# Performance work log

Measured on AMD Instinct MI355X. Metric: run time of the kernel, lower is better.

Reference implementation:

```python
import jax, jax.numpy as jnp
import numpy as np

N, D, K = 500_000, 64, 512

def setup_inputs() -> dict:
    key = jax.random.key(0)
    k1, k2, k3 = jax.random.split(key, 3)
    X = jax.random.normal(k1, (N, D), dtype=jnp.float32)
    centroids = jax.random.normal(k2, (K, D), dtype=jnp.float32)
    sample_weight = jax.random.uniform(k3, (N, D), dtype=jnp.float32)
    return {"X": X, "centroids": centroids, "sample_weight": sample_weight}

def reference(X, centroids, sample_weight):
    k, d = centroids.shape
    XX = jnp.sum(X * X, axis=1, keepdims=True)              # (N,1)
    CC = jnp.sum(centroids * centroids, axis=1)[None, :]    # (1,K)  == _centroid_sum
    Xc = X @ centroids.T                                    # (N,K)
    distances = jnp.sqrt(jnp.clip(XX - 2.0 * Xc + CC, 0.0) / d)
    y_hat = jnp.argmin(distances, axis=1)                   # hard assignment
    inertia = jnp.sum(jnp.min(distances, axis=1))           # summarize() return value
    # scatter_add_ accumulation of sufficient statistics
    w_sum = jax.ops.segment_sum(sample_weight, y_hat, num_segments=k)        # (K,D)
    xw_sum = jax.ops.segment_sum(X * sample_weight, y_hat, num_segments=k)   # (K,D)
    # pack outputs into a single array: rows [0:K]=xw_sum, [K:2K]=w_sum, last row=inertia
    return jnp.concatenate([xw_sum, w_sum, jnp.broadcast_to(inertia / d, (1, d)) * 0 + inertia[None if False else ...] if False else jnp.broadcast_to(inertia, (1, d))], axis=0)
```

## Files before the change

kernel.cpp:

```cpp
#include <hip/hip_runtime.h>
#include <hip/hip_bf16.h>


#define D_DIM 64
#define K_CLUS 512
#define RPT 128
#define AGRID_MAX 1024
#define SEGROWS 64

typedef __attribute__((ext_vector_type(8))) short short8;
typedef __attribute__((ext_vector_type(4))) float f32x4;

__device__ inline void barrier_lds_only() {
    asm volatile("s_waitcnt lgkmcnt(0)\n\ts_barrier" ::: "memory");
}

__device__ inline float dot4sq(float4 a) {
    return a.x * a.x + a.y * a.y + a.z * a.z + a.w * a.w;
}
__device__ inline unsigned short bfb(float f) {
    unsigned int u = __float_as_uint(f);
    return (unsigned short)((u + 0x7FFFu + ((u >> 16) & 1u)) >> 16);
}
__device__ inline short8 pack8f(float4 a, float4 b) {
    union { short8 s; __hip_bfloat162 q[4]; } r;
    r.q[0] = __float22bfloat162_rn(make_float2(a.x, a.y));
    r.q[1] = __float22bfloat162_rn(make_float2(a.z, a.w));
    r.q[2] = __float22bfloat162_rn(make_float2(b.x, b.y));
    r.q[3] = __float22bfloat162_rn(make_float2(b.z, b.w));
    return r.s;
}
__device__ inline float bfhi(unsigned u) { return __uint_as_float(u & 0xFFFF0000u); }
__device__ inline float bflo(unsigned u) { return __uint_as_float(u << 16); }

__global__ void cc_kernel(const float* __restrict__ C, float* __restrict__ CChalf,
                          unsigned short* __restrict__ Cb, int k_total) {
    int k = blockIdx.x * blockDim.x + threadIdx.x;
    if (k >= k_total) return;
    const float4* cp = (const float4*)(C + (size_t)k * D_DIM);
    unsigned short* ob = Cb + (size_t)k * D_DIM;
    float s = 0.f;
#pragma unroll
    for (int i = 0; i < 16; ++i) {
        float4 c = cp[i];
        s += dot4sq(c);
        ob[4 * i + 0] = bfb(c.x); ob[4 * i + 1] = bfb(c.y);
        ob[4 * i + 2] = bfb(c.z); ob[4 * i + 3] = bfb(c.w);
    }
    CChalf[k] = 0.5f * s;
}

__global__ __launch_bounds__(512, 4) void assign_mfma(
        const float* __restrict__ X, const unsigned short* __restrict__ Cb,
        const float* __restrict__ CChalf, int* __restrict__ y,
        int* __restrict__ lrank, int* __restrict__ baseTab,
        int* __restrict__ count, float* __restrict__ inertia_ws,
        uint4* __restrict__ X16, int n, int ntiles) {
    __shared__ __align__(16) char xb_lds[RPT * 128];
    __shared__ __align__(16) unsigned int partial[RPT][8];
    __shared__ float xs_lds[2][RPT];
    __shared__ int lhist[K_CLUS];

    int tid = threadIdx.x;
    lhist[tid] = 0;

    int lane = tid & 63, wid = tid >> 6;
    int c15 = lane & 15, g = lane >> 4;
    int wbase = wid * 64;

    short8 cf0[4], cf1[4];
    f32x4 nc[4];
#pragma unroll
    for (int ct = 0; ct < 4; ++ct) {
        const char* cp = (const char*)(Cb + (size_t)(wbase + ct * 16 + c15) * D_DIM);
        cf0[ct] = *(const short8*)(cp + (g << 4));
        cf1[ct] = *(const short8*)(cp + 64 + (g << 4));
#pragma unroll
        for (int r2 = 0; r2 < 4; ++r2)
            nc[ct][r2] = -CChalf[wbase + ct * 16 + (g << 2) + r2];
    }

    int srow = tid >> 3;
    int sb = (tid & 7) << 4;
    int sf = (tid & 7) << 3;
    unsigned swz = ((unsigned)(srow & 7)) << 4;

    float4 a0 = {0,0,0,0}, a1 = {0,0,0,0}, b0 = {0,0,0,0}, b1 = {0,0,0,0};
    int tile = blockIdx.x;
    if (tile < ntiles) {
        int rA = min(tile * RPT + srow, n - 1);
        int rB = min(tile * RPT + 64 + srow, n - 1);
        const float4* xa = (const float4*)(X + (size_t)rA * D_DIM + sf);
        const float4* xb = (const float4*)(X + (size_t)rB * D_DIM + sf);
        a0 = xa[0]; a1 = xa[1]; b0 = xb[0]; b1 = xb[1];
    }
    float iner = 0.f;
    int it = 0;

    for (; tile < ntiles; tile += gridDim.x, ++it) {
        int par = it & 1;
        int rA = min(tile * RPT + srow, n - 1);
        int rB = min(tile * RPT + 64 + srow, n - 1);
        short8 pA = pack8f(a0, a1);
        short8 pB = pack8f(b0, b1);
        *(short8*)(xb_lds + (srow << 7) + (sb ^ swz)) = pA;
        *(short8*)(xb_lds + ((64 + srow) << 7) + (sb ^ swz)) = pB;
        float psA = dot4sq(a0) + dot4sq(a1);
        float psB = dot4sq(b0) + dot4sq(b1);
        psA += __shfl_xor(psA, 1); psA += __shfl_xor(psA, 2); psA += __shfl_xor(psA, 4);
        psB += __shfl_xor(psB, 1); psB += __shfl_xor(psB, 2); psB += __shfl_xor(psB, 4);
        if ((tid & 7) == 0) {
            xs_lds[par][srow] = psA;
            xs_lds[par][64 + srow] = psB;
        }
        barrier_lds_only();

        union { short8 s8; uint4 u4; } cA, cB;
        cA.s8 = pA; cB.s8 = pB;
        X16[(size_t)rA * 8 + (tid & 7)] = cA.u4;
        X16[(size_t)rB * 8 + (tid & 7)] = cB.u4;

        int ntile = tile + gridDim.x;
        if (ntile < ntiles) {
            int nA = min(ntile * RPT + srow, n - 1);
            int nB = min(ntile * RPT + 64 + srow, n - 1);
            const float4* xa = (const float4*)(X + (size_t)nA * D_DIM + sf);
            const float4* xb = (const float4*)(X + (size_t)nB * D_DIM + sf);
            a0 = xa[0]; a1 = xa[1]; b0 = xb[0]; b1 = xb[1];
        }

#pragma unroll
        for (int s = 0; s < 8; ++s) {
            int arow = s * 16 + c15;
            const char* ab = xb_lds + (arow << 7);
            unsigned asw = ((unsigned)(arow & 7)) << 4;
            short8 xa = *(const short8*)(ab + ((g << 4) ^ asw));
            short8 xbv = *(const short8*)(ab + ((64 + (g << 4)) ^ asw));

            float best = -3.4e38f;
            int bpos = 0;
#pragma unroll
            for (int ct = 0; ct < 4; ++ct) {
                f32x4 acc = __builtin_amdgcn_mfma_f32_16x16x32_bf16(cf0[ct], xa, nc[ct], 0, 0, 0);
                acc = __builtin_amdgcn_mfma_f32_16x16x32_bf16(cf1[ct], xbv, acc, 0, 0, 0);
                float sc0 = acc[0], sc1 = acc[1], sc2 = acc[2], sc3 = acc[3];
                bool b01 = sc1 > sc0;  float v01 = b01 ? sc1 : sc0;  int p01 = b01 ? 1 : 0;
                bool b23 = sc3 > sc2;  float v23 = b23 ? sc3 : sc2;  int p23 = b23 ? 3 : 2;
                bool bq  = v23 > v01;  float vq  = bq ? v23 : v01;   int pq  = bq ? p23 : p01;
                if (vq > best) { best = vq; bpos = (ct << 2) + pq; }
            }
            int kg = wbase + ((bpos >> 2) << 4) + (g << 2) + (bpos & 3);
            unsigned u = __float_as_uint(best);
            unsigned mono = u ^ ((u & 0x80000000u) ? 0xFFFFFFFFu : 0x80000000u);
            unsigned key = (mono & 0xFFFFFE00u) | ((unsigned)kg ^ 0x1FFu);
            unsigned o = (unsigned)__shfl_xor((int)key, 16); key = key > o ? key : o;
            o = (unsigned)__shfl_xor((int)key, 32); key = key > o ? key : o;
            if (g == 0) partial[s * 16 + c15][wid] = key;
        }
        barrier_lds_only();

        if (tid < RPT) {
            int grow = tile * RPT + tid;
            if (grow < n) {
                const uint4* pp = (const uint4*)&partial[tid][0];
                uint4 p0 = pp[0], p1 = pp[1];
                unsigned key = p0.x;
                key = key > p0.y ? key : p0.y;
                key = key > p0.z ? key : p0.z;
                key = key > p0.w ? key : p0.w;
                key = key > p1.x ? key : p1.x;
                key = key > p1.y ? key : p1.y;
                key = key > p1.z ? key : p1.z;
                key = key > p1.w ? key : p1.w;
                int kg = (int)((key & 0x1FFu) ^ 0x1FFu);
                unsigned m2 = (key & 0xFFFFFE00u) | 0x100u;
                unsigned ub = (m2 & 0x80000000u) ? (m2 ^ 0x80000000u) : ~m2;
                float sbest = __uint_as_float(ub);
                float xx = xs_lds[par][tid];
                y[grow] = kg;
                lrank[grow] = atomicAdd(&lhist[kg], 1);
                iner += sqrtf(fmaxf(xx - 2.f * sbest, 0.f) * (1.0f / 64.0f));
            }
        }
    }

    __syncthreads();
    int b = atomicAdd(count + tid, lhist[tid]);
    baseTab[blockIdx.x * K_CLUS + tid] = b;

    if (wid < 2) {
#pragma unroll
        for (int off = 1; off < 64; off <<= 1) iner += __shfl_xor(iner, off);
        if (lane == 0) atomicAdd(inertia_ws, iner);
    }
}

__global__ __launch_bounds__(K_CLUS) void prefix_kernel(
        const int* __restrict__ count, int* __restrict__ offset,
        int* __restrict__ segKS, int* __restrict__ segmeta) {
    __shared__ int tmp[K_CLUS];
    __shared__ int tns[K_CLUS];
    int t = threadIdx.x;
    int c = count[t];
    int ns = (c + SEGROWS - 1) / SEGROWS;
    tmp[t] = c; tns[t] = ns;
    __syncthreads();
    for (int s = 1; s < K_CLUS; s <<= 1) {
        int v1 = (t >= s) ? tmp[t - s] : 0;
        int v2 = (t >= s) ? tns[t - s] : 0;
        __syncthreads();
        tmp[t] += v1; tns[t] += v2;
        __syncthreads();
    }
    offset[t] = tmp[t] - c;
    int so = tns[t] - ns;
    for (int s = 0; s < ns; ++s) segKS[so + s] = (t << 16) | s;
    if (t == K_CLUS - 1) segmeta[0] = tns[t];
}

__global__ __launch_bounds__(256) void scatter_kernel(
        const int* __restrict__ y, const int* __restrict__ lrank,
        const int* __restrict__ offset, const int* __restrict__ baseTab,
        int* __restrict__ sorted, int n, int agrid) {
    int row = blockIdx.x * blockDim.x + threadIdx.x;
    if (row >= n) return;
    int k = y[row];
    int blk = (row / RPT) % agrid;
    sorted[offset[k] + baseTab[blk * K_CLUS + k] + lrank[row]] = row;
}

__global__ __launch_bounds__(256, 6) void cluster_accum_v3(
        const uint4* __restrict__ X16, const float* __restrict__ W,
        const int* __restrict__ sorted, const int* __restrict__ offset,
        const int* __restrict__ count, const int* __restrict__ segKS,
        const int* __restrict__ segmeta, float* __restrict__ out) {
    int bid = blockIdx.x;
    if (bid >= segmeta[0]) return;
    int v = segKS[bid];
    int k = v >> 16, s = v & 0xFFFF;
    int cnt = count[k];
    int lo = s * SEGROWS;
    int m = min(cnt - lo, SEGROWS);
    int start = offset[k] + lo;
    int lane = threadIdx.x & 63, w = threadIdx.x >> 6;
    int grp = (w << 2) | (lane >> 4);
    int l8 = lane & 7;
    int h = (lane >> 3) & 1;
    int g4 = grp * 4;
    const float4* W4 = (const float4*)W;

    int i0 = g4 + h;
    int i1 = g4 + 2 + h;
    int r0 = (i0 < m) ? sorted[start + i0] : -1;
    int r1 = (i1 < m) ? sorted[start + i1] : -1;

    uint4 zz = {0u, 0u, 0u, 0u};
    float4 fz = {0.f, 0.f, 0.f, 0.f};
    uint4 xq0 = zz, xq1 = zz;
    float4 wa0 = fz, wb0 = fz, wa1 = fz, wb1 = fz;
    if (r0 >= 0) {
        xq0 = X16[(size_t)r0 * 8 + l8];
        wa0 = W4[(size_t)r0 * 16 + 2 * l8];
        wb0 = W4[(size_t)r0 * 16 + 2 * l8 + 1];
    }
    if (r1 >= 0) {
        xq1 = X16[(size_t)r1 * 8 + l8];
        wa1 = W4[(size_t)r1 * 16 + 2 * l8];
        wb1 = W4[(size_t)r1 * 16 + 2 * l8 + 1];
    }

    float axw[8], aww[8];
#pragma unroll
    for (int j = 0; j < 8; ++j) { axw[j] = 0.f; aww[j] = 0.f; }

#pragma unroll
    for (int r = 0; r < 2; ++r) {
        uint4 xq = r ? xq1 : xq0;
        float4 wa = r ? wa1 : wa0;
        float4 wb = r ? wb1 : wb0;
        float xf[8];
        xf[0] = bflo(xq.x); xf[1] = bfhi(xq.x);
        xf[2] = bflo(xq.y); xf[3] = bfhi(xq.y);
        xf[4] = bflo(xq.z); xf[5] = bfhi(xq.z);
        xf[6] = bflo(xq.w); xf[7] = bfhi(xq.w);
        axw[0] = fmaf(xf[0], wa.x, axw[0]); aww[0] += wa.x;
        axw[1] = fmaf(xf[1], wa.y, axw[1]); aww[1] += wa.y;
        axw[2] = fmaf(xf[2], wa.z, axw[2]); aww[2] += wa.z;
        axw[3] = fmaf(xf[3], wa.w, axw[3]); aww[3] += wa.w;
        axw[4] = fmaf(xf[4], wb.x, axw[4]); aww[4] += wb.x;
        axw[5] = fmaf(xf[5], wb.y, axw[5]); aww[5] += wb.y;
        axw[6] = fmaf(xf[6], wb.z, axw[6]); aww[6] += wb.z;
        axw[7] = fmaf(xf[7], wb.w, axw[7]); aww[7] += wb.w;
    }
#pragma unroll
    for (int j = 0; j < 8; ++j) {
        axw[j] += __shfl_xor(axw[j], 8);
        aww[j] += __shfl_xor(aww[j], 8);
    }

    __shared__ float sxw[16][D_DIM];
    __shared__ float sww[16][D_DIM];
    if (h == 0) {
#pragma unroll
        for (int j = 0; j < 8; ++j) {
            sxw[grp][8 * l8 + j] = axw[j];
            sww[grp][8 * l8 + j] = aww[j];
        }
    }
    __syncthreads();
    int t = threadIdx.x;
    if (t < 128) {
        int half = t >> 6, d = t & 63;
        const float(*src)[D_DIM] = half ? sww : sxw;
        float acc = 0.f;
#pragma unroll
        for (int jg = 0; jg < 16; ++jg) acc += src[jg][d];
        atomicAdd(out + (size_t)(half ? K_CLUS + k : k) * D_DIM + d, acc);
    }
}

__global__ void finalize_kernel(const float* __restrict__ inertia_ws, float* __restrict__ out) {
    out[(size_t)(2 * K_CLUS) * D_DIM + threadIdx.x] = *inertia_ws;
}

__global__ __launch_bounds__(256) void assign_scalar(
        const float* __restrict__ X, const float* __restrict__ C,
        const float* __restrict__ CChalf, int* __restrict__ y,
        int* __restrict__ count, float* __restrict__ inertia_ws, int n) {
    int row = blockIdx.x * blockDim.x + threadIdx.x;
    float mind = 0.f;
    if (row < n) {
        float4 x[16];
        const float4* xp = (const float4*)(X + (size_t)row * D_DIM);
#pragma unroll
        for (int i = 0; i < 16; ++i) x[i] = xp[i];
        float xx = 0.f;
#pragma unroll
        for (int i = 0; i < 16; ++i) xx += dot4sq(x[i]);
        float best = -3.4e38f;
        int bestk = 0;
        for (int k = 0; k < K_CLUS; ++k) {
            const float4* cp = (const float4*)(C + (size_t)k * D_DIM);
            float s0 = 0.f;
#pragma unroll
            for (int i = 0; i < 16; ++i) {
                float4 c = cp[i];
                s0 += x[i].x * c.x + x[i].y * c.y + x[i].z * c.z + x[i].w * c.w;
            }
            float sc = s0 - CChalf[k];
            if (sc > best) { best = sc; bestk = k; }
        }
        y[row] = bestk;
        atomicAdd(&count[bestk], 1);
        mind = sqrtf(fmaxf(xx - 2.f * best, 0.f) * (1.0f / 64.0f));
    }
    float s = mind;
#pragma unroll
    for (int off = 32; off > 0; off >>= 1) s += __shfl_xor(s, off);
    __shared__ float wsum[4];
    int w = threadIdx.x >> 6;
    if ((threadIdx.x & 63) == 0) wsum[w] = s;
    __syncthreads();
    if (threadIdx.x == 0)
        atomicAdd(inertia_ws, wsum[0] + wsum[1] + wsum[2] + wsum[3]);
}

__global__ __launch_bounds__(256) void accum_atomic_kernel(
        const float* __restrict__ X, const float* __restrict__ W,
        const int* __restrict__ y, float* __restrict__ out, int n) {
    int row = blockIdx.x * blockDim.x + threadIdx.x;
    if (row >= n) return;
    int k = y[row];
    const float4* xp = (const float4*)(X + (size_t)row * D_DIM);
    const float4* wp = (const float4*)(W + (size_t)row * D_DIM);
    float* xw = out + (size_t)k * D_DIM;
    float* wsv = out + (size_t)(K_CLUS + k) * D_DIM;
#pragma unroll
    for (int i = 0; i < 16; ++i) {
        float4 x = xp[i];
        float4 wq = wp[i];
        atomicAdd(xw + 4 * i + 0, x.x * wq.x);
        atomicAdd(xw + 4 * i + 1, x.y * wq.y);
        atomicAdd(xw + 4 * i + 2, x.z * wq.z);
        atomicAdd(xw + 4 * i + 3, x.w * wq.w);
        atomicAdd(wsv + 4 * i + 0, wq.x);
        atomicAdd(wsv + 4 * i + 1, wq.y);
        atomicAdd(wsv + 4 * i + 2, wq.z);
        atomicAdd(wsv + 4 * i + 3, wq.w);
    }
}

extern "C" void kernel_launch(void* const* d_in, const int* in_sizes, int n_in,
                              void* d_out, int out_size, void* d_ws, size_t ws_size,
                              hipStream_t stream) {
    const float* X = (const float*)d_in[0];
    const float* C = (const float*)d_in[1];
    const float* W = (const float*)d_in[2];
    float* out = (float*)d_out;
    int n = in_sizes[0] / D_DIM;
    int k_total = in_sizes[1] / D_DIM;

    int nsegmax = k_total + (n + SEGROWS - 1) / SEGROWS;
    int nblk = (n + 255) / 256;
    int ntiles = (n + RPT - 1) / RPT;
    int agrid = ntiles < AGRID_MAX ? ntiles : AGRID_MAX;

    char* ws = (char*)d_ws;
    int*            count   = (int*)ws;
    float*          inertia = (float*)(ws + 2048);
    int*            segmeta = (int*)(ws + 2056);
    float*          cchalf  = (float*)(ws + 2560);
    int*            offset  = (int*)(ws + 8192);
    unsigned short* Cb      = (unsigned short*)(ws + 12288);

    size_t base = 81920;
    size_t x16_bytes = (size_t)n * 128;
    size_t full_tab  = base + x16_bytes;
    size_t needed_full = full_tab + (size_t)n * 12 +
                         (size_t)AGRID_MAX * K_CLUS * 4 + (size_t)nsegmax * 4;

    hipMemsetAsync(ws, 0, 4096, stream);
    hipMemsetAsync(d_out, 0, (size_t)out_size * sizeof(float), stream);
    cc_kernel<<<(k_total + 255) / 256, 256, 0, stream>>>(C, cchalf, Cb, k_total);

    if (ws_size >= needed_full) {
        uint4* X16    = (uint4*)(ws + base);
        int* yv       = (int*)(ws + full_tab);
        int* lrank    = (int*)(ws + full_tab + (size_t)n * 4);
        int* sorted   = (int*)(ws + full_tab + (size_t)n * 8);
        int* baseTab  = (int*)(ws + full_tab + (size_t)n * 12);
        int* segKS    = (int*)(ws + full_tab + (size_t)n * 12 +
                               (size_t)AGRID_MAX * K_CLUS * 4);
        assign_mfma<<<agrid, 512, 0, stream>>>(X, Cb, cchalf, yv, lrank, baseTab,
                                               count, inertia, X16, n, ntiles);
        prefix_kernel<<<1, K_CLUS, 0, stream>>>(count, offset, segKS, segmeta);
        scatter_kernel<<<nblk, 256, 0, stream>>>(yv, lrank, offset, baseTab, sorted, n, agrid);
        cluster_accum_v3<<<nsegmax, 256, 0, stream>>>(X16, W, sorted, offset, count,
                                                      segKS, segmeta, out);
        finalize_kernel<<<1, D_DIM, 0, stream>>>(inertia, out);
    } else {
        int* yv = (int*)(ws + base);
        assign_scalar<<<nblk, 256, 0, stream>>>(X, C, cchalf, yv, count, inertia, n);
        accum_atomic_kernel<<<nblk, 256, 0, stream>>>(X, W, yv, out, n);
        finalize_kernel<<<1, D_DIM, 0, stream>>>(inertia, out);
    }
}
```

Baseline: 131.3 us.

## Fold memsets and finalize into kernels, add dynamic tile scheduling in assign

Memsets of the workspace and output are moved into extra blocks of the centroid-prep kernel, and the inertia write is folded into the prefix kernel, removing two memset launches and one kernel launch. The assign kernel now fetches tiles from a global atomic work counter and records each tile's owner block for the scatter kernel, which balances load across blocks. The final per-row reduction is spread over one 16-lane group per wave instead of the first 128 threads. This adds atomics per tile and an extra owner table lookup.

```diff
diff --git a/kernel.cpp b/kernel.cpp
--- a/kernel.cpp
+++ b/kernel.cpp
@@ -33,21 +33,34 @@
 __device__ inline float bfhi(unsigned u) { return __uint_as_float(u & 0xFFFF0000u); }
 __device__ inline float bflo(unsigned u) { return __uint_as_float(u << 16); }
 
-__global__ void cc_kernel(const float* __restrict__ C, float* __restrict__ CChalf,
-                          unsigned short* __restrict__ Cb, int k_total) {
-    int k = blockIdx.x * blockDim.x + threadIdx.x;
-    if (k >= k_total) return;
-    const float4* cp = (const float4*)(C + (size_t)k * D_DIM);
-    unsigned short* ob = Cb + (size_t)k * D_DIM;
-    float s = 0.f;
-#pragma unroll
-    for (int i = 0; i < 16; ++i) {
-        float4 c = cp[i];
-        s += dot4sq(c);
-        ob[4 * i + 0] = bfb(c.x); ob[4 * i + 1] = bfb(c.y);
-        ob[4 * i + 2] = bfb(c.z); ob[4 * i + 3] = bfb(c.w);
-    }
-    CChalf[k] = 0.5f * s;
+__global__ __launch_bounds__(256) void cc_kernel(
+        const float* __restrict__ C, float* __restrict__ CChalf,
+        unsigned short* __restrict__ Cb, int k_total,
+        int* __restrict__ wspage, float* __restrict__ out, int out_sz) {
+    int b = blockIdx.x, tid = threadIdx.x;
+    if (b < 2) {
+        int k = b * 256 + tid;
+        if (k >= k_total) return;
+        const float4* cp = (const float4*)(C + (size_t)k * D_DIM);
+        unsigned short* ob = Cb + (size_t)k * D_DIM;
+        float s = 0.f;
+#pragma unroll
+        for (int i = 0; i < 16; ++i) {
+            float4 c = cp[i];
+            s += dot4sq(c);
+            ob[4 * i + 0] = bfb(c.x); ob[4 * i + 1] = bfb(c.y);
+            ob[4 * i + 2] = bfb(c.z); ob[4 * i + 3] = bfb(c.w);
+        }
+        CChalf[k] = 0.5f * s;
+    } else if (b == 2) {
+        int4 z = {0, 0, 0, 0};
+        ((int4*)wspage)[tid] = z;
+    } else {
+        float4 z = {0.f, 0.f, 0.f, 0.f};
+        float4* o4 = (float4*)out;
+        int n4 = out_sz >> 2;
+        for (int i = (b - 3) * 256 + tid; i < n4; i += 768) o4[i] = z;
+    }
 }
 
 __global__ __launch_bounds__(512, 4) void assign_mfma(
@@ -55,14 +68,20 @@
         const float* __restrict__ CChalf, int* __restrict__ y,
         int* __restrict__ lrank, int* __restrict__ baseTab,
         int* __restrict__ count, float* __restrict__ inertia_ws,
-        uint4* __restrict__ X16, int n, int ntiles) {
+        uint4* __restrict__ X16, int* __restrict__ workctr,
+        int* __restrict__ tileOwner, int n, int ntiles) {
     __shared__ __align__(16) char xb_lds[RPT * 128];
     __shared__ __align__(16) unsigned int partial[RPT][8];
     __shared__ float xs_lds[2][RPT];
     __shared__ int lhist[K_CLUS];
+    __shared__ int idq[4];
 
     int tid = threadIdx.x;
     lhist[tid] = 0;
+    if (tid == 0) {
+        idq[0] = atomicAdd(workctr, 1);
+        idq[1] = atomicAdd(workctr, 1);
+    }
 
     int lane = tid & 63, wid = tid >> 6;
     int c15 = lane & 15, g = lane >> 4;
@@ -85,8 +104,10 @@
     int sf = (tid & 7) << 3;
     unsigned swz = ((unsigned)(srow & 7)) << 4;
 
+    __syncthreads();
+    int tile = idq[0], tnext = idq[1];
+
     float4 a0 = {0,0,0,0}, a1 = {0,0,0,0}, b0 = {0,0,0,0}, b1 = {0,0,0,0};
-    int tile = blockIdx.x;
     if (tile < ntiles) {
         int rA = min(tile * RPT + srow, n - 1);
         int rB = min(tile * RPT + 64 + srow, n - 1);
@@ -97,7 +118,7 @@
     float iner = 0.f;
     int it = 0;
 
-    for (; tile < ntiles; tile += gridDim.x, ++it) {
+    while (tile < ntiles) {
         int par = it & 1;
         int rA = min(tile * RPT + srow, n - 1);
         int rB = min(tile * RPT + 64 + srow, n - 1);
@@ -115,15 +136,19 @@
         }
         barrier_lds_only();
 
+        if (tid == 0) {
+            tileOwner[tile] = blockIdx.x;
+            idq[(it + 2) & 3] = atomicAdd(workctr, 1);
+        }
+
         union { short8 s8; uint4 u4; } cA, cB;
         cA.s8 = pA; cB.s8 = pB;
         X16[(size_t)rA * 8 + (tid & 7)] = cA.u4;
         X16[(size_t)rB * 8 + (tid & 7)] = cB.u4;
 
-        int ntile = tile + gridDim.x;
-        if (ntile < ntiles) {
-            int nA = min(ntile * RPT + srow, n - 1);
-            int nB = min(ntile * RPT + 64 + srow, n - 1);
+        if (tnext < ntiles) {
+            int nA = min(tnext * RPT + srow, n - 1);
+            int nB = min(tnext * RPT + 64 + srow, n - 1);
             const float4* xa = (const float4*)(X + (size_t)nA * D_DIM + sf);
             const float4* xb = (const float4*)(X + (size_t)nB * D_DIM + sf);
             a0 = xa[0]; a1 = xa[1]; b0 = xb[0]; b1 = xb[1];
@@ -159,10 +184,11 @@
         }
         barrier_lds_only();
 
-        if (tid < RPT) {
-            int grow = tile * RPT + tid;
+        if ((lane >> 4) == 0) {
+            int r = (wid << 4) + c15;
+            int grow = tile * RPT + r;
             if (grow < n) {
-                const uint4* pp = (const uint4*)&partial[tid][0];
+                const uint4* pp = (const uint4*)&partial[r][0];
                 uint4 p0 = pp[0], p1 = pp[1];
                 unsigned key = p0.x;
                 key = key > p0.y ? key : p0.y;
@@ -176,28 +202,30 @@
                 unsigned m2 = (key & 0xFFFFFE00u) | 0x100u;
                 unsigned ub = (m2 & 0x80000000u) ? (m2 ^ 0x80000000u) : ~m2;
                 float sbest = __uint_as_float(ub);
-                float xx = xs_lds[par][tid];
+                float xx = xs_lds[par][r];
                 y[grow] = kg;
                 lrank[grow] = atomicAdd(&lhist[kg], 1);
                 iner += sqrtf(fmaxf(xx - 2.f * sbest, 0.f) * (1.0f / 64.0f));
             }
         }
+        tile = tnext;
+        tnext = idq[(it + 2) & 3];
+        ++it;
     }
 
     __syncthreads();
     int b = atomicAdd(count + tid, lhist[tid]);
     baseTab[blockIdx.x * K_CLUS + tid] = b;
 
-    if (wid < 2) {
-#pragma unroll
-        for (int off = 1; off < 64; off <<= 1) iner += __shfl_xor(iner, off);
-        if (lane == 0) atomicAdd(inertia_ws, iner);
-    }
+#pragma unroll
+    for (int off = 1; off < 64; off <<= 1) iner += __shfl_xor(iner, off);
+    if (lane == 0) atomicAdd(inertia_ws, iner);
 }
 
 __global__ __launch_bounds__(K_CLUS) void prefix_kernel(
         const int* __restrict__ count, int* __restrict__ offset,
-        int* __restrict__ segKS, int* __restrict__ segmeta) {
+        int* __restrict__ segKS, int* __restrict__ segmeta,
+        const float* __restrict__ inertia_ws, float* __restrict__ out) {
     __shared__ int tmp[K_CLUS];
     __shared__ int tns[K_CLUS];
     int t = threadIdx.x;
@@ -216,16 +244,17 @@
     int so = tns[t] - ns;
     for (int s = 0; s < ns; ++s) segKS[so + s] = (t << 16) | s;
     if (t == K_CLUS - 1) segmeta[0] = tns[t];
+    if (t < D_DIM) out[(size_t)(2 * K_CLUS) * D_DIM + t] = *inertia_ws;
 }
 
 __global__ __launch_bounds__(256) void scatter_kernel(
         const int* __restrict__ y, const int* __restrict__ lrank,
         const int* __restrict__ offset, const int* __restrict__ baseTab,
-        int* __restrict__ sorted, int n, int agrid) {
+        const int* __restrict__ tileOwner, int* __restrict__ sorted, int n) {
     int row = blockIdx.x * blockDim.x + threadIdx.x;
     if (row >= n) return;
     int k = y[row];
-    int blk = (row / RPT) % agrid;
+    int blk = tileOwner[row >> 7];
     sorted[offset[k] + baseTab[blk * K_CLUS + k] + lrank[row]] = row;
 }
 
@@ -409,6 +438,7 @@
     int*            count   = (int*)ws;
     float*          inertia = (float*)(ws + 2048);
     int*            segmeta = (int*)(ws + 2056);
+    int*            workctr = (int*)(ws + 2060);
     float*          cchalf  = (float*)(ws + 2560);
     int*            offset  = (int*)(ws + 8192);
     unsigned short* Cb      = (unsigned short*)(ws + 12288);
@@ -416,12 +446,9 @@
     size_t base = 81920;
     size_t x16_bytes = (size_t)n * 128;
     size_t full_tab  = base + x16_bytes;
-    size_t needed_full = full_tab + (size_t)n * 12 +
-                         (size_t)AGRID_MAX * K_CLUS * 4 + (size_t)nsegmax * 4;
-
-    hipMemsetAsync(ws, 0, 4096, stream);
-    hipMemsetAsync(d_out, 0, (size_t)out_size * sizeof(float), stream);
-    cc_kernel<<<(k_total + 255) / 256, 256, 0, stream>>>(C, cchalf, Cb, k_total);
+    size_t ownoff    = full_tab + (size_t)n * 12 +
+                       (size_t)AGRID_MAX * K_CLUS * 4 + (size_t)nsegmax * 4;
+    size_t needed_full = ownoff + (size_t)ntiles * 4;
 
     if (ws_size >= needed_full) {
         uint4* X16    = (uint4*)(ws + base);
@@ -431,15 +458,25 @@
         int* baseTab  = (int*)(ws + full_tab + (size_t)n * 12);
         int* segKS    = (int*)(ws + full_tab + (size_t)n * 12 +
                                (size_t)AGRID_MAX * K_CLUS * 4);
+        int* tileOwner = (int*)(ws + ownoff);
+
+        cc_kernel<<<6, 256, 0, stream>>>(C, cchalf, Cb, k_total,
+                                         (int*)ws, out, out_size);
         assign_mfma<<<agrid, 512, 0, stream>>>(X, Cb, cchalf, yv, lrank, baseTab,
-                                               count, inertia, X16, n, ntiles);
-        prefix_kernel<<<1, K_CLUS, 0, stream>>>(count, offset, segKS, segmeta);
-        scatter_kernel<<<nblk, 256, 0, stream>>>(yv, lrank, offset, baseTab, sorted, n, agrid);
+                                               count, inertia, X16, workctr,
+                                               tileOwner, n, ntiles);
+        prefix_kernel<<<1, K_CLUS, 0, stream>>>(count, offset, segKS, segmeta,
+                                                inertia, out);
+        scatter_kernel<<<nblk, 256, 0, stream>>>(yv, lrank, offset, baseTab,
+                                                 tileOwner, sorted, n);
         cluster_accum_v3<<<nsegmax, 256, 0, stream>>>(X16, W, sorted, offset, count,
                                                       segKS, segmeta, out);
-        finalize_kernel<<<1, D_DIM, 0, stream>>>(inertia, out);
     } else {
         int* yv = (int*)(ws + base);
+        hipMemsetAsync(ws, 0, 4096, stream);
+        hipMemsetAsync(d_out, 0, (size_t)out_size * sizeof(float), stream);
+        cc_kernel<<<6, 256, 0, stream>>>(C, cchalf, Cb, k_total,
+                                         (int*)ws, out, out_size);
         assign_scalar<<<nblk, 256, 0, stream>>>(X, C, cchalf, yv, count, inertia, n);
         accum_atomic_kernel<<<nblk, 256, 0, stream>>>(X, W, yv, out, n);
         finalize_kernel<<<1, D_DIM, 0, stream>>>(inertia, out);
```

Measured after the change: 238.8 us. 1.82x slower.
